# Performance work log

Hardware: AMD Instinct MI355X
Metric: run time of the kernel (lower is better)

The kernel has to match this reference:

```python
import jax, jax.numpy as jnp
import numpy as np

HEAD_DIM = 128
KS = 3          # kernel_size
DIL = 1         # dilation
SCALE = HEAD_DIM ** (-0.5)  # qk_scale defaults to head_dim**-0.5


def _unfold(x, ks, dil):
    # Equivalent of nn.Unfold(ks, dil, pad=dil*(ks-1)//2, stride=1), reshaped to
    # [B, d, ks*ks, H, W] (torch's C-major-then-kernel ordering matches stacking
    # kernel offsets on a new axis after the channel axis).
    B, d, H, W = x.shape
    p = dil * (ks - 1) // 2
    xp = jnp.pad(x, ((0, 0), (0, 0), (p, p), (p, p)))
    patches = [xp[:, :, i * dil:i * dil + H, j * dil:j * dil + W]
               for i in range(ks) for j in range(ks)]
    return jnp.stack(patches, axis=2)  # [B, d, ks*ks, H, W]


def setup_inputs() -> dict:
    key = jax.random.key(0)
    k1, k2, k3 = jax.random.split(key, 3)
    shape = (32, HEAD_DIM, 64, 64)
    return {
        "q": jax.random.normal(k1, shape, dtype=jnp.float32),
        "k": jax.random.normal(k2, shape, dtype=jnp.float32),
        "v": jax.random.normal(k3, shape, dtype=jnp.float32),
    }


def reference(q, k, v):
    # Local (unfold) branch: dilation=1 < 5.
    kk = _unfold(k, KS, DIL)                                   # [B,d,9,H,W]
    logits = jnp.einsum('bdhw,bdkhw->bkhw', q, kk) * SCALE     # per-pixel q @ k_window
    attn = jax.nn.softmax(logits, axis=1)                      # softmax over 9 neighbors
    vv = _unfold(v, KS, DIL)                                   # [B,d,9,H,W]
    x = jnp.einsum('bkhw,bdkhw->bhwd', attn, vv)               # [B,H,W,d]
    return x
```

## Files before the change

### kernel.cpp

```cpp
#include <hip/hip_runtime.h>

static constexpr int HD   = 128;
static constexpr int HH   = 64;
static constexpr int WW   = 64;
static constexpr int ROWS = 2;
static constexpr int BLK  = 512;
static constexpr int HALO = ROWS + 2;
static constexpr int DC   = 16;
static constexpr int NCH  = HD / DC;
static constexpr int LSTR = 16;
static constexpr float SCALE = 0.08838834764831845f;

__global__ __launch_bounds__(BLK, 4) void natten3_kernel(
    const float* __restrict__ Q, const float* __restrict__ K,
    const float* __restrict__ V, float* __restrict__ O)
{
  __shared__ float buf[2][HALO * WW * LSTR];

  const int tid = threadIdx.x;
  const int qf  = tid & 3;
  const int px  = tid >> 2;
  const int w   = px & 63;
  const int pr  = px >> 6;

  const int bid = blockIdx.x;
  const int swz = (bid & 7) * 128 + (bid >> 3);
  const int b   = swz >> 5;
  const int h0  = (swz & 31) * ROWS;
  const int hh  = h0 + pr;

  const int plane = HH * WW;
  const size_t img = (size_t)HD * plane;
  const float* Qb = Q + (size_t)b * img;
  const float* Kb = K + (size_t)b * img;
  const float* Vb = V + (size_t)b * img;
  const int qoff = hh * WW + w;
  const int dq   = 4 * qf;

  int sg_g[2], sg_l[2];
  #pragma unroll
  for (int it = 0; it < 2; ++it) {
    const int idx  = it * BLK + tid;
    const int ws   = idx & 63;
    const int rest = idx >> 6;
    const int is   = rest >> 2;
    const int gs   = rest & 3;
    const int grow = min(max(h0 - 1 + is, 0), HH - 1);
    sg_g[it] = gs * 4 * plane + grow * WW + ws;
    sg_l[it] = (is * WW + ws) * LSTR + 4 * (gs ^ ((ws >> 2) & 3));
  }

  int   lofs[9];
  float msk[9];
  #pragma unroll
  for (int dh = 0; dh < 3; ++dh) {
    #pragma unroll
    for (int dw = 0; dw < 3; ++dw) {
      const int j = dh * 3 + dw;
      const int r = hh + dh - 1, c = w + dw - 1;
      msk[j] = (r >= 0 && r < HH && c >= 0 && c < WW) ? 1.0f : 0.0f;
      const int cc = min(max(c, 0), WW - 1);
      lofs[j] = ((pr + dh) * WW + cc) * LSTR + 4 * (qf ^ ((cc >> 2) & 3));
    }
  }

  {
    float s[2][4];
    #pragma unroll
    for (int it = 0; it < 2; ++it)
      #pragma unroll
      for (int p = 0; p < 4; ++p)
        s[it][p] = Kb[sg_g[it] + p * plane];
    #pragma unroll
    for (int it = 0; it < 2; ++it)
      *(float4*)&buf[0][sg_l[it]] = make_float4(s[it][0], s[it][1], s[it][2], s[it][3]);
  }
  float q[4];
  #pragma unroll
  for (int p = 0; p < 4; ++p) q[p] = Qb[(dq + p) * plane + qoff];
  __syncthreads();

  float logit[9];
  #pragma unroll
  for (int j = 0; j < 9; ++j) logit[j] = 0.0f;

  for (int c = 0; c < NCH; ++c) {
    const int cur = c & 1;
    float s[2][4], qn[4];
    if (c + 1 < NCH) {
      const int dbase = (c + 1) * DC * plane;
      #pragma unroll
      for (int it = 0; it < 2; ++it)
        #pragma unroll
        for (int p = 0; p < 4; ++p)
          s[it][p] = Kb[dbase + sg_g[it] + p * plane];
      #pragma unroll
      for (int p = 0; p < 4; ++p)
        qn[p] = Qb[((c + 1) * DC + dq + p) * plane + qoff];
    }
    const float* __restrict__ bc = buf[cur];
    #pragma unroll
    for (int j = 0; j < 9; ++j) {
      const float4 k4 = *(const float4*)&bc[lofs[j]];
      float acc = logit[j];
      acc = fmaf(q[0], k4.x, acc); acc = fmaf(q[1], k4.y, acc);
      acc = fmaf(q[2], k4.z, acc); acc = fmaf(q[3], k4.w, acc);
      logit[j] = acc;
    }
    if (c + 1 < NCH) {
      #pragma unroll
      for (int it = 0; it < 2; ++it)
        *(float4*)&buf[cur ^ 1][sg_l[it]] = make_float4(s[it][0], s[it][1], s[it][2], s[it][3]);
      #pragma unroll
      for (int p = 0; p < 4; ++p) q[p] = qn[p];
    }
    __syncthreads();
  }

  float vs[2][4];
  #pragma unroll
  for (int it = 0; it < 2; ++it)
    #pragma unroll
    for (int p = 0; p < 4; ++p)
      vs[it][p] = Vb[sg_g[it] + p * plane];

  #pragma unroll
  for (int j = 0; j < 9; ++j) {
    logit[j] += __shfl_xor(logit[j], 1);
    logit[j] += __shfl_xor(logit[j], 2);
  }
  #pragma unroll
  for (int j = 0; j < 9; ++j) logit[j] = msk[j] * logit[j] * SCALE;
  float m = logit[0];
  #pragma unroll
  for (int j = 1; j < 9; ++j) m = fmaxf(m, logit[j]);
  float att[9];
  float Z = 0.0f;
  #pragma unroll
  for (int j = 0; j < 9; ++j) { att[j] = __expf(logit[j] - m); Z += att[j]; }
  const float rZ = 1.0f / Z;
  #pragma unroll
  for (int j = 0; j < 9; ++j) att[j] *= rZ * msk[j];

  #pragma unroll
  for (int it = 0; it < 2; ++it)
    *(float4*)&buf[0][sg_l[it]] = make_float4(vs[it][0], vs[it][1], vs[it][2], vs[it][3]);
  __syncthreads();

  const size_t obase = ((size_t)b * plane + (size_t)h0 * WW) * HD;
  float oprev[4];
  for (int c = 0; c < NCH; ++c) {
    const int cur = c & 1;
    float s[2][4];
    if (c + 1 < NCH) {
      const int dbase = (c + 1) * DC * plane;
      #pragma unroll
      for (int it = 0; it < 2; ++it)
        #pragma unroll
        for (int p = 0; p < 4; ++p)
          s[it][p] = Vb[dbase + sg_g[it] + p * plane];
    }
    float o0 = 0.f, o1 = 0.f, o2 = 0.f, o3 = 0.f;
    const float* __restrict__ bc = buf[cur];
    #pragma unroll
    for (int j = 0; j < 9; ++j) {
      const float4 v4 = *(const float4*)&bc[lofs[j]];
      const float a = att[j];
      o0 = fmaf(a, v4.x, o0); o1 = fmaf(a, v4.y, o1);
      o2 = fmaf(a, v4.z, o2); o3 = fmaf(a, v4.w, o3);
    }
    if (c & 1) {
      const size_t oa = obase + (size_t)px * HD + (size_t)(c - 1) * DC + dq;
      *(float4*)&O[oa]      = make_float4(oprev[0], oprev[1], oprev[2], oprev[3]);
      *(float4*)&O[oa + DC] = make_float4(o0, o1, o2, o3);
    } else {
      oprev[0] = o0; oprev[1] = o1; oprev[2] = o2; oprev[3] = o3;
    }
    if (c + 1 < NCH) {
      #pragma unroll
      for (int it = 0; it < 2; ++it)
        *(float4*)&buf[cur ^ 1][sg_l[it]] = make_float4(s[it][0], s[it][1], s[it][2], s[it][3]);
      __syncthreads();
    }
  }
}

extern "C" void kernel_launch(void* const* d_in, const int* in_sizes, int n_in,
                              void* d_out, int out_size, void* d_ws, size_t ws_size,
                              hipStream_t stream) {
  const float* q = (const float*)d_in[0];
  const float* k = (const float*)d_in[1];
  const float* v = (const float*)d_in[2];
  float* o = (float*)d_out;
  const int nblocks = 32 * (HH / ROWS);
  natten3_kernel<<<dim3(nblocks), dim3(BLK), 0, stream>>>(q, k, v, o);
}
```

Baseline: 42.89 us.

## Unify K and V tile streaming into one deeper-prefetch pipeline with custom barriers

```diff
diff --git a/kernel.cpp b/kernel.cpp
--- a/kernel.cpp
+++ b/kernel.cpp
@@ -8,8 +8,11 @@
 static constexpr int HALO = ROWS + 2;
 static constexpr int DC   = 16;
 static constexpr int NCH  = HD / DC;
+static constexpr int NT   = 16;
 static constexpr int LSTR = 16;
 static constexpr float SCALE = 0.08838834764831845f;
+
+#define MEMFENCE asm volatile("" ::: "memory")
 
 __global__ __launch_bounds__(BLK, 4) void natten3_kernel(
     const float* __restrict__ Q, const float* __restrict__ K,
@@ -50,55 +53,45 @@
     sg_l[it] = (is * WW + ws) * LSTR + 4 * (gs ^ ((ws >> 2) & 3));
   }
 
-  int   lofs[9];
-  float msk[9];
-  #pragma unroll
-  for (int dh = 0; dh < 3; ++dh) {
+  int lofs[9];
+  #pragma unroll
+  for (int dh = 0; dh < 3; ++dh)
     #pragma unroll
     for (int dw = 0; dw < 3; ++dw) {
-      const int j = dh * 3 + dw;
-      const int r = hh + dh - 1, c = w + dw - 1;
-      msk[j] = (r >= 0 && r < HH && c >= 0 && c < WW) ? 1.0f : 0.0f;
-      const int cc = min(max(c, 0), WW - 1);
-      lofs[j] = ((pr + dh) * WW + cc) * LSTR + 4 * (qf ^ ((cc >> 2) & 3));
-    }
-  }
-
-  {
-    float s[2][4];
+      const int cc = min(max(w + dw - 1, 0), WW - 1);
+      lofs[dh * 3 + dw] = ((pr + dh) * WW + cc) * LSTR + 4 * (qf ^ ((cc >> 2) & 3));
+    }
+
+  auto LOADS = [&](float* s, int t) {
+    const float* cb = (t < NCH ? Kb : Vb) + (t & 7) * DC * plane;
     #pragma unroll
     for (int it = 0; it < 2; ++it)
       #pragma unroll
       for (int p = 0; p < 4; ++p)
-        s[it][p] = Kb[sg_g[it] + p * plane];
-    #pragma unroll
-    for (int it = 0; it < 2; ++it)
-      *(float4*)&buf[0][sg_l[it]] = make_float4(s[it][0], s[it][1], s[it][2], s[it][3]);
-  }
-  float q[4];
-  #pragma unroll
-  for (int p = 0; p < 4; ++p) q[p] = Qb[(dq + p) * plane + qoff];
-  __syncthreads();
-
+        s[it * 4 + p] = cb[sg_g[it] + p * plane];
+  };
+  auto LOADQ = [&](float* qq, int c) {
+    #pragma unroll
+    for (int p = 0; p < 4; ++p)
+      qq[p] = Qb[(c * DC + dq + p) * plane + qoff];
+  };
+  auto WRITE = [&](int slot, const float* s) {
+    *(float4*)&buf[slot][sg_l[0]] = make_float4(s[0], s[1], s[2], s[3]);
+    *(float4*)&buf[slot][sg_l[1]] = make_float4(s[4], s[5], s[6], s[7]);
+  };
+  auto BAR = [&]() {
+    asm volatile("s_waitcnt lgkmcnt(0)" ::: "memory");
+    __builtin_amdgcn_s_barrier();
+    MEMFENCE;
+  };
+
+  float sA[8], sB[8], q[4], qn[4];
   float logit[9];
   #pragma unroll
   for (int j = 0; j < 9; ++j) logit[j] = 0.0f;
 
-  for (int c = 0; c < NCH; ++c) {
-    const int cur = c & 1;
-    float s[2][4], qn[4];
-    if (c + 1 < NCH) {
-      const int dbase = (c + 1) * DC * plane;
-      #pragma unroll
-      for (int it = 0; it < 2; ++it)
-        #pragma unroll
-        for (int p = 0; p < 4; ++p)
-          s[it][p] = Kb[dbase + sg_g[it] + p * plane];
-      #pragma unroll
-      for (int p = 0; p < 4; ++p)
-        qn[p] = Qb[((c + 1) * DC + dq + p) * plane + qoff];
-    }
-    const float* __restrict__ bc = buf[cur];
+  auto COMPK = [&](int slot) {
+    const float* __restrict__ bc = buf[slot];
     #pragma unroll
     for (int j = 0; j < 9; ++j) {
       const float4 k4 = *(const float4*)&bc[lofs[j]];
@@ -107,80 +100,103 @@
       acc = fmaf(q[2], k4.z, acc); acc = fmaf(q[3], k4.w, acc);
       logit[j] = acc;
     }
-    if (c + 1 < NCH) {
-      #pragma unroll
-      for (int it = 0; it < 2; ++it)
-        *(float4*)&buf[cur ^ 1][sg_l[it]] = make_float4(s[it][0], s[it][1], s[it][2], s[it][3]);
+  };
+
+  LOADS(sA, 0);
+  LOADQ(q, 0);
+  LOADS(sB, 1);
+  MEMFENCE;
+  WRITE(0, sA);
+  BAR();
+
+  #pragma unroll 1
+  for (int c = 0; c < NCH; c += 2) {
+    LOADS(sA, c + 2);
+    LOADQ(qn, c + 1);
+    MEMFENCE;
+    COMPK(0);
+    WRITE(1, sB);
+    #pragma unroll
+    for (int p = 0; p < 4; ++p) q[p] = qn[p];
+    BAR();
+    LOADS(sB, c + 3);
+    if (c + 2 < NCH) LOADQ(qn, c + 2);
+    MEMFENCE;
+    COMPK(1);
+    WRITE(0, sA);
+    if (c + 2 < NCH) {
       #pragma unroll
       for (int p = 0; p < 4; ++p) q[p] = qn[p];
     }
-    __syncthreads();
-  }
-
-  float vs[2][4];
-  #pragma unroll
-  for (int it = 0; it < 2; ++it)
-    #pragma unroll
-    for (int p = 0; p < 4; ++p)
-      vs[it][p] = Vb[sg_g[it] + p * plane];
+    BAR();
+  }
 
   #pragma unroll
   for (int j = 0; j < 9; ++j) {
     logit[j] += __shfl_xor(logit[j], 1);
     logit[j] += __shfl_xor(logit[j], 2);
   }
-  #pragma unroll
-  for (int j = 0; j < 9; ++j) logit[j] = msk[j] * logit[j] * SCALE;
-  float m = logit[0];
-  #pragma unroll
-  for (int j = 1; j < 9; ++j) m = fmaxf(m, logit[j]);
   float att[9];
-  float Z = 0.0f;
-  #pragma unroll
-  for (int j = 0; j < 9; ++j) { att[j] = __expf(logit[j] - m); Z += att[j]; }
-  const float rZ = 1.0f / Z;
-  #pragma unroll
-  for (int j = 0; j < 9; ++j) att[j] *= rZ * msk[j];
-
-  #pragma unroll
-  for (int it = 0; it < 2; ++it)
-    *(float4*)&buf[0][sg_l[it]] = make_float4(vs[it][0], vs[it][1], vs[it][2], vs[it][3]);
-  __syncthreads();
+  {
+    float msk[9];
+    #pragma unroll
+    for (int dh = 0; dh < 3; ++dh)
+      #pragma unroll
+      for (int dw = 0; dw < 3; ++dw) {
+        const int j = dh * 3 + dw;
+        const int r = hh + dh - 1, c = w + dw - 1;
+        msk[j] = (r >= 0 && r < HH && c >= 0 && c < WW) ? 1.0f : 0.0f;
+      }
+    #pragma unroll
+    for (int j = 0; j < 9; ++j) logit[j] = msk[j] * logit[j] * SCALE;
+    float m = logit[0];
+    #pragma unroll
+    for (int j = 1; j < 9; ++j) m = fmaxf(m, logit[j]);
+    float Z = 0.0f;
+    #pragma unroll
+    for (int j = 0; j < 9; ++j) { att[j] = __expf(logit[j] - m); Z += att[j]; }
+    const float rZ = 1.0f / Z;
+    #pragma unroll
+    for (int j = 0; j < 9; ++j) att[j] *= rZ * msk[j];
+  }
 
   const size_t obase = ((size_t)b * plane + (size_t)h0 * WW) * HD;
-  float oprev[4];
-  for (int c = 0; c < NCH; ++c) {
-    const int cur = c & 1;
-    float s[2][4];
-    if (c + 1 < NCH) {
-      const int dbase = (c + 1) * DC * plane;
-      #pragma unroll
-      for (int it = 0; it < 2; ++it)
-        #pragma unroll
-        for (int p = 0; p < 4; ++p)
-          s[it][p] = Vb[dbase + sg_g[it] + p * plane];
-    }
-    float o0 = 0.f, o1 = 0.f, o2 = 0.f, o3 = 0.f;
-    const float* __restrict__ bc = buf[cur];
-    #pragma unroll
-    for (int j = 0; j < 9; ++j) {
-      const float4 v4 = *(const float4*)&bc[lofs[j]];
-      const float a = att[j];
-      o0 = fmaf(a, v4.x, o0); o1 = fmaf(a, v4.y, o1);
-      o2 = fmaf(a, v4.z, o2); o3 = fmaf(a, v4.w, o3);
-    }
-    if (c & 1) {
-      const size_t oa = obase + (size_t)px * HD + (size_t)(c - 1) * DC + dq;
-      *(float4*)&O[oa]      = make_float4(oprev[0], oprev[1], oprev[2], oprev[3]);
-      *(float4*)&O[oa + DC] = make_float4(o0, o1, o2, o3);
-    } else {
-      oprev[0] = o0; oprev[1] = o1; oprev[2] = o2; oprev[3] = o3;
-    }
-    if (c + 1 < NCH) {
-      #pragma unroll
-      for (int it = 0; it < 2; ++it)
-        *(float4*)&buf[cur ^ 1][sg_l[it]] = make_float4(s[it][0], s[it][1], s[it][2], s[it][3]);
-      __syncthreads();
+  #pragma unroll 1
+  for (int t = NCH; t < NT; t += 2) {
+    float oA0 = 0.f, oA1 = 0.f, oA2 = 0.f, oA3 = 0.f;
+    float oB0 = 0.f, oB1 = 0.f, oB2 = 0.f, oB3 = 0.f;
+    if (t + 2 < NT) LOADS(sA, t + 2);
+    MEMFENCE;
+    {
+      const float* __restrict__ bc = buf[0];
+      #pragma unroll
+      for (int j = 0; j < 9; ++j) {
+        const float4 v4 = *(const float4*)&bc[lofs[j]];
+        const float a = att[j];
+        oA0 = fmaf(a, v4.x, oA0); oA1 = fmaf(a, v4.y, oA1);
+        oA2 = fmaf(a, v4.z, oA2); oA3 = fmaf(a, v4.w, oA3);
+      }
+    }
+    WRITE(1, sB);
+    BAR();
+    if (t + 3 < NT) LOADS(sB, t + 3);
+    MEMFENCE;
+    {
+      const float* __restrict__ bc = buf[1];
+      #pragma unroll
+      for (int j = 0; j < 9; ++j) {
+        const float4 v4 = *(const float4*)&bc[lofs[j]];
+        const float a = att[j];
+        oB0 = fmaf(a, v4.x, oB0); oB1 = fmaf(a, v4.y, oB1);
+        oB2 = fmaf(a, v4.z, oB2); oB3 = fmaf(a, v4.w, oB3);
+      }
+    }
+    const size_t oa = obase + (size_t)px * HD + (size_t)(t - NCH) * DC + dq;
+    *(float4*)&O[oa]      = make_float4(oA0, oA1, oA2, oA3);
+    *(float4*)&O[oa + DC] = make_float4(oB0, oB1, oB2, oB3);
+    if (t + 2 < NT) {
+      WRITE(0, sA);
+      BAR();
     }
   }
 }
```

Result: slower. 66.57 us (+55.2%).
